# Optimization experiments

Hardware: AMD Instinct MI355X
Metric: run time of the kernel (lower is better)

The kernel has to match this reference:

```python
import jax, jax.numpy as jnp
import numpy as np

N_SAMPLES, N_NODES, IN_CH, HID, OUT_CH = 262144, 24, 32, 32, 1

def setup_inputs() -> dict:
    key = jax.random.key(0)
    k = jax.random.split(key, 6)
    h = jax.random.normal(k[0], (N_SAMPLES, N_NODES, IN_CH), dtype=jnp.float32)
    valid = jax.random.randint(k[1], (N_SAMPLES, N_NODES), 0, 2, dtype=jnp.int32)
    # per-node MLP params, PyTorch-style init scale ~ 1/sqrt(fan_in)
    W1 = jax.random.normal(k[2], (N_NODES, IN_CH, HID), dtype=jnp.float32) / np.sqrt(IN_CH)
    b1 = jax.random.normal(k[3], (N_NODES, HID), dtype=jnp.float32) / np.sqrt(IN_CH)
    W2 = jax.random.normal(k[4], (N_NODES, HID, OUT_CH), dtype=jnp.float32) / np.sqrt(HID)
    b2 = jax.random.normal(k[5], (N_NODES, OUT_CH), dtype=jnp.float32) / np.sqrt(HID)
    return {"h": h, "valid": valid, "W1": W1, "b1": b1, "W2": W2, "b2": b2}

def reference(h, valid, W1, b1, W2, b2):
    # Per-node MLP: input ReLU -> Linear(in,W) -> ReLU -> Linear(W,out).
    # Instead of a Python loop with gather/scatter over nodes, run all
    # nodes as a batched (grouped) GEMM and mask invalid entries to zero
    # (the torch code leaves invalid slots at their zero init).
    x = jax.nn.relu(h)                                    # [S, N, C]
    x = jax.nn.relu(jnp.einsum('snc,ncw->snw', x, W1) + b1[None])  # [S, N, W]
    out = jnp.einsum('snw,nwo->sno', x, W2) + b2[None]    # [S, N, O]
    mask = (valid > 0)[:, :, None]                        # [S, N, 1]
    return jnp.where(mask, out, jnp.zeros((), out.dtype))
```

## Files before the change

### kernel.cpp

```cpp
#include <hip/hip_runtime.h>

#define NS   262144
#define NN   24
#define CI   32
#define HW   32
#define SPB  16
#define NTILES (NS / SPB)
#define NBLK 256
#define TPB  (NTILES / NBLK)

typedef __fp16 fp16x2v __attribute__((ext_vector_type(2)));
typedef _Float16 half8 __attribute__((ext_vector_type(8)));
typedef float f32x4 __attribute__((ext_vector_type(4)));
typedef unsigned int u32x4 __attribute__((ext_vector_type(4)));

__device__ alignas(16) unsigned short g_w1f[NN * 2 * 64 * 8];

__global__ void pack_w1(const float* __restrict__ W1) {
  int idx = blockIdx.x * 256 + threadIdx.x;
  if (idx >= NN * 2 * 64 * 8) return;
  int i    = idx & 7;
  int lane = (idx >> 3) & 63;
  int hf   = (idx >> 9) & 1;
  int n    = idx >> 10;
  int k = (lane >> 4) * 8 + i;
  int w = hf * 16 + (lane & 15);
  _Float16 v = (_Float16)W1[(n * CI + k) * HW + w];
  g_w1f[idx] = __builtin_bit_cast(unsigned short, v);
}

__device__ __forceinline__ unsigned pkrtz(float a, float b) {
  fp16x2v p = __builtin_amdgcn_cvt_pkrtz(a, b);
  return __builtin_bit_cast(unsigned, p);
}

__device__ __forceinline__ void gload16(const float* g, float* l) {
  __builtin_amdgcn_global_load_lds(
      (const __attribute__((address_space(1))) void*)g,
      (__attribute__((address_space(3))) void*)l, 16, 0, 0);
}

__global__ __launch_bounds__(512, 2) void mlp_mfma(
    const float* __restrict__ h, const int* __restrict__ valid,
    const float* __restrict__ b1, const float* __restrict__ W2,
    const float* __restrict__ b2, float* __restrict__ out) {
  __shared__ alignas(16) float buf[2][SPB * NN * CI];
  __shared__ float sb1[NN * HW], sw2[NN * HW], sb2v[NN];

  const int tid  = threadIdx.x;
  const int lane = tid & 63;
  const int wv   = tid >> 6;
  const int r    = lane & 15;
  const int q    = lane >> 4;

  {
    const int t4 = tid * 4;
    if (t4 < NN * HW) {
      *(f32x4*)&sb1[t4] = *(const f32x4*)&b1[t4];
      *(f32x4*)&sw2[t4] = *(const f32x4*)&W2[t4];
    }
    if (tid < NN) sb2v[tid] = b2[tid];
  }

  half8 Af0[3], Af1[3];
#pragma unroll
  for (int ni = 0; ni < 3; ++ni) {
    const int n = wv * 3 + ni;
    Af0[ni] = __builtin_bit_cast(half8,
        *(const u32x4*)&g_w1f[((n * 2 + 0) * 64 + lane) * 8]);
    Af1[ni] = __builtin_bit_cast(half8,
        *(const u32x4*)&g_w1f[((n * 2 + 1) * 64 + lane) * 8]);
  }

  const int tile0 = blockIdx.x * TPB;

#define STAGE(tile, dst)                                                      \
  do {                                                                        \
    const float* gt = h + (size_t)(tile) * (SPB * NN * CI);                   \
    _Pragma("unroll") for (int rd = 0; rd < 6; ++rd) {                        \
      const int k2 = rd * 8 + wv;                                             \
      const int s  = k2 / 3, third = k2 % 3;                                  \
      const int dstf = (k2 * 64 + lane) * 4;            \
      const int srcb = ((third * 64 + lane) * 16) ^ ((s & 7) << 4);           \
      gload16(gt + s * 768 + (srcb >> 2), (dst) + dstf);                      \
    }                                                                         \
  } while (0)

  STAGE(tile0, buf[0]);
  __syncthreads();

  const int aA = r * 3072 + ((q * 32) ^ ((r & 7) << 4));
  const int aB = aA ^ 16;

  for (int t = 0; t < TPB; ++t) {
    const char* cb = (const char*)buf[t & 1];

    if (t + 1 < TPB) STAGE(tile0 + t + 1, buf[(t + 1) & 1]);

    const int srow = (tile0 + t) * SPB + r;

#pragma unroll
    for (int ni = 0; ni < 3; ++ni) {
      const int n = wv * 3 + ni;
      f32x4 d0 = *(const f32x4*)(cb + aA + n * 128);
      f32x4 d1 = *(const f32x4*)(cb + aB + n * 128);

      int vld = 0;
      if (lane < 16) vld = valid[srow * NN + n];

      u32x4 uu;
      uu[0] = pkrtz(fmaxf(d0[0], 0.f), fmaxf(d0[1], 0.f));
      uu[1] = pkrtz(fmaxf(d0[2], 0.f), fmaxf(d0[3], 0.f));
      uu[2] = pkrtz(fmaxf(d1[0], 0.f), fmaxf(d1[1], 0.f));
      uu[3] = pkrtz(fmaxf(d1[2], 0.f), fmaxf(d1[3], 0.f));
      half8 Hf = __builtin_bit_cast(half8, uu);

      f32x4 b1a = *(const f32x4*)&sb1[n * HW + q * 4];
      f32x4 b1b = *(const f32x4*)&sb1[n * HW + 16 + q * 4];
      f32x4 w2a = *(const f32x4*)&sw2[n * HW + q * 4];
      f32x4 w2b = *(const f32x4*)&sw2[n * HW + 16 + q * 4];

      f32x4 c0 = {b1a[0], b1a[1], b1a[2], b1a[3]};
      f32x4 c1 = {b1b[0], b1b[1], b1b[2], b1b[3]};
      c0 = __builtin_amdgcn_mfma_f32_16x16x32_f16(Af0[ni], Hf, c0, 0, 0, 0);
      c1 = __builtin_amdgcn_mfma_f32_16x16x32_f16(Af1[ni], Hf, c1, 0, 0, 0);

      float p = 0.f;
#pragma unroll
      for (int i = 0; i < 4; ++i) {
        p = fmaf(fmaxf(c0[i], 0.f), w2a[i], p);
        p = fmaf(fmaxf(c1[i], 0.f), w2b[i], p);
      }
      p += __shfl_xor(p, 16);
      p += __shfl_xor(p, 32);

      if (lane < 16)
        out[(size_t)srow * NN + n] = vld ? (p + sb2v[n]) : 0.0f;
    }

    __syncthreads();
  }
#undef STAGE
}

extern "C" void kernel_launch(void* const* d_in, const int* in_sizes, int n_in,
                              void* d_out, int out_size, void* d_ws, size_t ws_size,
                              hipStream_t stream) {
  const float* h     = (const float*)d_in[0];
  const int*   valid = (const int*)d_in[1];
  const float* W1    = (const float*)d_in[2];
  const float* b1    = (const float*)d_in[3];
  const float* W2    = (const float*)d_in[4];
  const float* b2    = (const float*)d_in[5];
  float* out = (float*)d_out;

  hipLaunchKernelGGL(pack_w1, dim3((NN * 2 * 64 * 8 + 255) / 256), dim3(256),
                     0, stream, W1);
  hipLaunchKernelGGL(mlp_mfma, dim3(NBLK), dim3(512), 0, stream,
                     h, valid, b1, W2, b2, out);
}
```

Measured before the change: 217.6 us.

## Triple-buffer h tiles with explicit vmcnt waits and raw barriers

Moves from double to triple buffering of the staged h tiles in LDS, prefetching two tiles ahead. Full __syncthreads are replaced with precise s_waitcnt vmcnt counts plus s_barrier, so outstanding global loads (including valid loads and stores) need not fully drain each iteration. The valid load is now unconditional across all lanes. This aims to hide global-memory latency better, at the cost of more LDS (which may lower occupancy at 2 blocks per CU) and fragile hand-counted vmcnt values that must match the number of issued memory ops.

```diff
diff --git a/kernel.cpp b/kernel.cpp
--- a/kernel.cpp
+++ b/kernel.cpp
@@ -44,7 +44,7 @@
     const float* __restrict__ h, const int* __restrict__ valid,
     const float* __restrict__ b1, const float* __restrict__ W2,
     const float* __restrict__ b2, float* __restrict__ out) {
-  __shared__ alignas(16) float buf[2][SPB * NN * CI];
+  __shared__ alignas(16) float buf[3][SPB * NN * CI];
   __shared__ float sb1[NN * HW], sw2[NN * HW], sb2v[NN];
 
   const int tid  = threadIdx.x;
@@ -80,67 +80,74 @@
     _Pragma("unroll") for (int rd = 0; rd < 6; ++rd) {                        \
       const int k2 = rd * 8 + wv;                                             \
       const int s  = k2 / 3, third = k2 % 3;                                  \
-      const int dstf = (k2 * 64 + lane) * 4;            \
+      const int dstf = (k2 * 64 + lane) * 4;                                  \
       const int srcb = ((third * 64 + lane) * 16) ^ ((s & 7) << 4);           \
       gload16(gt + s * 768 + (srcb >> 2), (dst) + dstf);                      \
     }                                                                         \
   } while (0)
 
-  STAGE(tile0, buf[0]);
-  __syncthreads();
-
   const int aA = r * 3072 + ((q * 32) ^ ((r & 7) << 4));
   const int aB = aA ^ 16;
 
-  for (int t = 0; t < TPB; ++t) {
-    const char* cb = (const char*)buf[t & 1];
+#define COMPUTE(t, src)                                                       \
+  do {                                                                        \
+    const char* cb = (const char*)(src);                                      \
+    const int srow = (tile0 + (t)) * SPB + r;                                 \
+    _Pragma("unroll") for (int ni = 0; ni < 3; ++ni) {                        \
+      const int n = wv * 3 + ni;                                              \
+      f32x4 d0 = *(const f32x4*)(cb + aA + n * 128);                          \
+      f32x4 d1 = *(const f32x4*)(cb + aB + n * 128);                          \
+      const int vld = valid[srow * NN + n];                                   \
+      u32x4 uu;                                                               \
+      uu[0] = pkrtz(fmaxf(d0[0], 0.f), fmaxf(d0[1], 0.f));                    \
+      uu[1] = pkrtz(fmaxf(d0[2], 0.f), fmaxf(d0[3], 0.f));                    \
+      uu[2] = pkrtz(fmaxf(d1[0], 0.f), fmaxf(d1[1], 0.f));                    \
+      uu[3] = pkrtz(fmaxf(d1[2], 0.f), fmaxf(d1[3], 0.f));                    \
+      half8 Hf = __builtin_bit_cast(half8, uu);                               \
+      f32x4 b1a = *(const f32x4*)&sb1[n * HW + q * 4];                        \
+      f32x4 b1b = *(const f32x4*)&sb1[n * HW + 16 + q * 4];                   \
+      f32x4 w2a = *(const f32x4*)&sw2[n * HW + q * 4];                        \
+      f32x4 w2b = *(const f32x4*)&sw2[n * HW + 16 + q * 4];                   \
+      f32x4 c0 = {b1a[0], b1a[1], b1a[2], b1a[3]};                            \
+      f32x4 c1 = {b1b[0], b1b[1], b1b[2], b1b[3]};                            \
+      c0 = __builtin_amdgcn_mfma_f32_16x16x32_f16(Af0[ni], Hf, c0, 0, 0, 0);  \
+      c1 = __builtin_amdgcn_mfma_f32_16x16x32_f16(Af1[ni], Hf, c1, 0, 0, 0);  \
+      float p = 0.f;                                                          \
+      _Pragma("unroll") for (int i = 0; i < 4; ++i) {                         \
+        p = fmaf(fmaxf(c0[i], 0.f), w2a[i], p);                               \
+        p = fmaf(fmaxf(c1[i], 0.f), w2b[i], p);                               \
+      }                                                                       \
+      p += __shfl_xor(p, 16);                                                 \
+      p += __shfl_xor(p, 32);                                                 \
+      if (lane < 16)                                                          \
+        out[(size_t)srow * NN + n] = vld ? (p + sb2v[n]) : 0.0f;              \
+    }                                                                         \
+  } while (0)
 
-    if (t + 1 < TPB) STAGE(tile0 + t + 1, buf[(t + 1) & 1]);
+  __syncthreads();
 
-    const int srow = (tile0 + t) * SPB + r;
+  STAGE(tile0 + 0, buf[0]);
+  STAGE(tile0 + 1, buf[1]);
+  asm volatile("s_waitcnt vmcnt(6)" ::: "memory");
+  __builtin_amdgcn_sched_barrier(0);
+  __builtin_amdgcn_s_barrier();
 
-#pragma unroll
-    for (int ni = 0; ni < 3; ++ni) {
-      const int n = wv * 3 + ni;
-      f32x4 d0 = *(const f32x4*)(cb + aA + n * 128);
-      f32x4 d1 = *(const f32x4*)(cb + aB + n * 128);
+  for (int t = 0; t < TPB - 2; ++t) {
+    COMPUTE(t, buf[t % 3]);
+    STAGE(tile0 + t + 2, buf[(t + 2) % 3]);
+    asm volatile("s_waitcnt vmcnt(10)" ::: "memory");
+    __builtin_amdgcn_sched_barrier(0);
+    __builtin_amdgcn_s_barrier();
+  }
 
-      int vld = 0;
-      if (lane < 16) vld = valid[srow * NN + n];
+  COMPUTE(TPB - 2, buf[(TPB - 2) % 3]);
+  asm volatile("s_waitcnt vmcnt(4)" ::: "memory");
+  __builtin_amdgcn_sched_barrier(0);
+  __builtin_amdgcn_s_barrier();
+  COMPUTE(TPB - 1, buf[(TPB - 1) % 3]);
 
-      u32x4 uu;
-      uu[0] = pkrtz(fmaxf(d0[0], 0.f), fmaxf(d0[1], 0.f));
-      uu[1] = pkrtz(fmaxf(d0[2], 0.f), fmaxf(d0[3], 0.f));
-      uu[2] = pkrtz(fmaxf(d1[0], 0.f), fmaxf(d1[1], 0.f));
-      uu[3] = pkrtz(fmaxf(d1[2], 0.f), fmaxf(d1[3], 0.f));
-      half8 Hf = __builtin_bit_cast(half8, uu);
-
-      f32x4 b1a = *(const f32x4*)&sb1[n * HW + q * 4];
-      f32x4 b1b = *(const f32x4*)&sb1[n * HW + 16 + q * 4];
-      f32x4 w2a = *(const f32x4*)&sw2[n * HW + q * 4];
-      f32x4 w2b = *(const f32x4*)&sw2[n * HW + 16 + q * 4];
-
-      f32x4 c0 = {b1a[0], b1a[1], b1a[2], b1a[3]};
-      f32x4 c1 = {b1b[0], b1b[1], b1b[2], b1b[3]};
-      c0 = __builtin_amdgcn_mfma_f32_16x16x32_f16(Af0[ni], Hf, c0, 0, 0, 0);
-      c1 = __builtin_amdgcn_mfma_f32_16x16x32_f16(Af1[ni], Hf, c1, 0, 0, 0);
-
-      float p = 0.f;
-#pragma unroll
-      for (int i = 0; i < 4; ++i) {
-        p = fmaf(fmaxf(c0[i], 0.f), w2a[i], p);
-        p = fmaf(fmaxf(c1[i], 0.f), w2b[i], p);
-      }
-      p += __shfl_xor(p, 16);
-      p += __shfl_xor(p, 32);
-
-      if (lane < 16)
-        out[(size_t)srow * NN + n] = vld ? (p + sb2v[n]) : 0.0f;
-    }
-
-    __syncthreads();
-  }
 #undef STAGE
+#undef COMPUTE
 }
 
 extern "C" void kernel_launch(void* const* d_in, const int* in_sizes, int n_in,
```

Result: faster. 212.3 us (-2.4%).
